# Kernel tuning notes

Hardware: AMD Instinct MI355X
Metric: run time of the kernel (lower is better)

## Reference

```python
import jax, jax.numpy as jnp
import numpy as np


def setup_inputs() -> dict:
    key = jax.random.key(0)
    k1, k2 = jax.random.split(key)
    N, D, C = 65536, 512, 64
    embeddings = jax.random.normal(k1, (N, D), dtype=jnp.float32)
    labels = jax.random.randint(k2, (N,), 0, C, dtype=jnp.int64)
    return {"embeddings": embeddings, "labels": labels, "num_classes": C}


def reference(embeddings, labels, num_classes):
    # Per-class mean (prototypes) via segment reductions. Labels are assumed
    # to be 0..C-1 with all classes present, so unique(labels) == arange(C)
    # and local_labels == labels (faithful to the torch loop in that regime).
    ones = jnp.ones(labels.shape, dtype=embeddings.dtype)
    counts = jax.ops.segment_sum(ones, labels, num_segments=num_classes)  # [C]
    sums = jax.ops.segment_sum(embeddings, labels, num_segments=num_classes)  # [C, D]
    prototypes = sums / counts[:, None]

    # Euclidean cdist: ||e||^2 + ||p||^2 - 2 e.p^T, clamped for numerical safety
    e2 = jnp.sum(embeddings * embeddings, axis=1, keepdims=True)  # [N, 1]
    p2 = jnp.sum(prototypes * prototypes, axis=1)  # [C]
    cross = embeddings @ prototypes.T  # [N, C]
    d2 = jnp.maximum(e2 + p2[None, :] - 2.0 * cross, 1e-12)
    logits = -jnp.sqrt(d2)  # [N, C], negative distances

    log_probs = jax.nn.log_softmax(logits, axis=1)
    n = labels.shape[0]
    nll = -log_probs[jnp.arange(n), labels]
    loss = jnp.mean(nll)
    accuracy = jnp.mean((jnp.argmax(logits, axis=1) == labels).astype(jnp.float32))
    return (loss, accuracy)
```

## Files before the change

kernel.cpp:

```cpp
#include <hip/hip_runtime.h>
#include <math.h>

#define NROWS 65536
#define DIM   512
#define NCLS  64
#define CCAP  1280

typedef __attribute__((ext_vector_type(4))) float f32x4;
typedef __attribute__((ext_vector_type(8))) short s16x8;

#define WS_PROTOSUM 0
#define WS_CURSORS  32768
#define WS_LOSS     32832
#define WS_ACC      32833
#define WS_DONE     32834
#define WS_P2       32836
#define WS_PERM     32912
#define WS_PBF      114944
#define WS_E2P      131328
#define WS_EBF      393472
#define WS_EXT_BYTES 68682752ULL
#define MEMSET_WORDS 32835

static __device__ __forceinline__ unsigned short f2bf(float f) {
    unsigned int u = __float_as_uint(f);
    u += 0x7FFF + ((u >> 16) & 1);
    return (unsigned short)(u >> 16);
}
static __device__ __forceinline__ float bf2f(unsigned short h) {
    return __uint_as_float(((unsigned int)h) << 16);
}

__global__ __launch_bounds__(256) void k_scatter(const int* __restrict__ labels,
                                                 int* __restrict__ cursors,
                                                 int* __restrict__ perm) {
    __shared__ int lh[NCLS], lb[NCLS];
    int t = threadIdx.x;
    if (t < NCLS) lh[t] = 0;
    __syncthreads();
    int i = blockIdx.x * 256 + t;
    int lab = labels[i];
    int rank = atomicAdd(&lh[lab], 1);
    __syncthreads();
    if (t < NCLS) lb[t] = atomicAdd(&cursors[t], lh[t]);
    __syncthreads();
    int pos = lb[lab] + rank;
    if (pos < CCAP) perm[lab * CCAP + pos] = i;
}

__global__ __launch_bounds__(256) void k_psumprep(const float* __restrict__ emb,
                                                  const int* __restrict__ cursors,
                                                  const int* __restrict__ perm,
                                                  float* __restrict__ protoSum,
                                                  unsigned short* __restrict__ ebf,
                                                  float* __restrict__ e2p) {
    __shared__ int permS[CCAP];
    __shared__ float4 red[256];
    int t   = threadIdx.x;
    int c   = blockIdx.x >> 5;
    int sub = blockIdx.x & 31;
    int dc  = sub & 3;
    int rs  = sub >> 2;
    int tl  = t & 31;
    int g   = t >> 5;

    int cnt = cursors[c];
    int n = (cnt < CCAP) ? cnt : CCAP;
    for (int i = t; i < n; i += 256) permS[i] = perm[c * CCAP + i];
    __syncthreads();

    const float4* eb = (const float4*)emb + dc * 32 + tl;
    float* e2o = e2p + (size_t)dc * NROWS;
    float4 acc = make_float4(0.f, 0.f, 0.f, 0.f);
#pragma unroll 2
    for (int i = rs * 8 + g; i < n; i += 64) {
        int r = permS[i];
        float4 v = eb[(size_t)r * 128];
        acc.x += v.x; acc.y += v.y; acc.z += v.z; acc.w += v.w;
        ushort4 h;
        h.x = f2bf(v.x); h.y = f2bf(v.y); h.z = f2bf(v.z); h.w = f2bf(v.w);
        *(ushort4*)(ebf + (size_t)r * DIM + dc * 128 + tl * 4) = h;
        float sq = v.x * v.x + v.y * v.y + v.z * v.z + v.w * v.w;
#pragma unroll
        for (int o = 1; o < 32; o <<= 1) sq += __shfl_xor(sq, o, 64);
        if (tl == 0) e2o[r] = sq;
    }
    red[t] = acc;
    __syncthreads();
    if (t < 32) {
        float4 s = red[t];
#pragma unroll
        for (int gg = 1; gg < 8; ++gg) {
            float4 v = red[gg * 32 + t];
            s.x += v.x; s.y += v.y; s.z += v.z; s.w += v.w;
        }
        float* dst = &protoSum[(size_t)c * DIM + dc * 128 + t * 4];
        atomicAdd(dst + 0, s.x);
        atomicAdd(dst + 1, s.y);
        atomicAdd(dst + 2, s.z);
        atomicAdd(dst + 3, s.w);
    }
}

__global__ __launch_bounds__(256) void k_psum(const float* __restrict__ emb,
                                              const int* __restrict__ cursors,
                                              const int* __restrict__ perm,
                                              float* __restrict__ protoSum) {
    __shared__ int permS[CCAP];
    __shared__ float4 red[256];
    int t   = threadIdx.x;
    int c   = blockIdx.x >> 5;
    int sub = blockIdx.x & 31;
    int dc  = sub & 3;
    int rs  = sub >> 2;
    int tl  = t & 31;
    int g   = t >> 5;

    int cnt = cursors[c];
    int n = (cnt < CCAP) ? cnt : CCAP;
    for (int i = t; i < n; i += 256) permS[i] = perm[c * CCAP + i];
    __syncthreads();

    const float4* eb = (const float4*)emb + dc * 32 + tl;
    float4 acc = make_float4(0.f, 0.f, 0.f, 0.f);
#pragma unroll 4
    for (int i = rs * 8 + g; i < n; i += 64) {
        int r = permS[i];
        float4 v = eb[(size_t)r * 128];
        acc.x += v.x; acc.y += v.y; acc.z += v.z; acc.w += v.w;
    }
    red[t] = acc;
    __syncthreads();
    if (t < 32) {
        float4 s = red[t];
#pragma unroll
        for (int gg = 1; gg < 8; ++gg) {
            float4 v = red[gg * 32 + t];
            s.x += v.x; s.y += v.y; s.z += v.z; s.w += v.w;
        }
        float* dst = &protoSum[(size_t)c * DIM + dc * 128 + t * 4];
        atomicAdd(dst + 0, s.x);
        atomicAdd(dst + 1, s.y);
        atomicAdd(dst + 2, s.z);
        atomicAdd(dst + 3, s.w);
    }
}

__global__ __launch_bounds__(512) void k_protofin(const float* __restrict__ protoSum,
                                                  const int* __restrict__ cursors,
                                                  unsigned short* __restrict__ pBf,
                                                  float* __restrict__ p2) {
    int c = blockIdx.x, d = threadIdx.x;
    float mean = protoSum[(size_t)c * DIM + d] / (float)cursors[c];
    unsigned short mb = f2bf(mean);
    int kc = d >> 5, quad = (d >> 3) & 3, j = d & 7;
    int nt = c >> 4, l15 = c & 15;
    pBf[(size_t)(((kc * 4 + quad) * 4 + nt) * 16 + l15) * 8 + j] = mb;
    float mf = bf2f(mb);
    float sq = mf * mf;
#pragma unroll
    for (int o = 32; o > 0; o >>= 1) sq += __shfl_down(sq, o, 64);
    __shared__ float red[8];
    if ((d & 63) == 0) red[d >> 6] = sq;
    __syncthreads();
    if (d == 0) {
        float ss = 0.f;
#pragma unroll
        for (int w = 0; w < 8; ++w) ss += red[w];
        p2[c] = ss;
    }
}

#define LROWS 64
#define LGRID (NROWS / LROWS)

__global__ __launch_bounds__(256, 4) void k_logits2(const unsigned short* __restrict__ ebf,
                                                 const float* __restrict__ e2p,
                                                 const int* __restrict__ labels,
                                                 const unsigned short* __restrict__ pBf,
                                                 const float* __restrict__ p2,
                                                 float* __restrict__ lossAcc,
                                                 float* __restrict__ accAcc,
                                                 unsigned int* __restrict__ doneCnt,
                                                 float* __restrict__ out) {
    __shared__ float rb[8];
    int t    = threadIdx.x;
    int lane = t & 63;
    int wv   = t >> 6;
    int quad = lane >> 4;
    int l15  = lane & 15;
    int rbase = blockIdx.x * LROWS;
    int row   = wv * 16 + l15;

    f32x4 acc[4];
#pragma unroll
    for (int nt = 0; nt < 4; ++nt) acc[nt] = (f32x4){0.f, 0.f, 0.f, 0.f};

    const s16x8* ap = (const s16x8*)(ebf + (size_t)(rbase + row) * DIM) + quad;
    const s16x8* bp = (const s16x8*)pBf + quad * 64 + l15;

#pragma unroll 4
    for (int kc = 0; kc < 16; ++kc) {
        s16x8 a = ap[kc * 4];
#pragma unroll
        for (int nt = 0; nt < 4; ++nt) {
            s16x8 b = bp[(size_t)kc * 256 + nt * 16];
            acc[nt] = __builtin_amdgcn_mfma_f32_16x16x32_bf16(a, b, acc[nt], 0, 0, 0);
        }
    }

    float nlls = 0.f, corr = 0.f;
#pragma unroll
    for (int reg = 0; reg < 4; ++reg) {
        int rloc = wv * 16 + quad * 4 + reg;
        int grow = rbase + rloc;
        float e2v = e2p[grow] + e2p[NROWS + grow]
                  + e2p[2 * NROWS + grow] + e2p[3 * NROWS + grow];
        float lg[4];
#pragma unroll
        for (int nt = 0; nt < 4; ++nt) {
            float d2 = e2v + p2[nt * 16 + l15] - 2.f * acc[nt][reg];
            d2 = fmaxf(d2, 1e-12f);
            lg[nt] = -sqrtf(d2);
        }
        float mv = lg[0]; int mc = l15;
#pragma unroll
        for (int nt = 1; nt < 4; ++nt) {
            int cix = nt * 16 + l15;
            if (lg[nt] > mv) { mv = lg[nt]; mc = cix; }
        }
#pragma unroll
        for (int o = 1; o < 16; o <<= 1) {
            float mo = __shfl_xor(mv, o, 64);
            int   co = __shfl_xor(mc, o, 64);
            if (mo > mv || (mo == mv && co < mc)) { mv = mo; mc = co; }
        }
        int lab = labels[grow];
        float se = 0.f, ll = 0.f;
#pragma unroll
        for (int nt = 0; nt < 4; ++nt) se += __expf(lg[nt] - mv);
        if ((lab & 15) == l15) ll = lg[lab >> 4];
#pragma unroll
        for (int o = 1; o < 16; o <<= 1) {
            se += __shfl_xor(se, o, 64);
            ll += __shfl_xor(ll, o, 64);
        }
        if (l15 == 0) {
            nlls += __logf(se) + mv - ll;
            corr += (mc == lab) ? 1.f : 0.f;
        }
    }
#pragma unroll
    for (int o = 1; o < 64; o <<= 1) {
        nlls += __shfl_xor(nlls, o, 64);
        corr += __shfl_xor(corr, o, 64);
    }
    if (lane == 0) { rb[wv] = nlls; rb[4 + wv] = corr; }
    __syncthreads();
    if (t == 0) {
        atomicAdd(lossAcc, rb[0] + rb[1] + rb[2] + rb[3]);
        atomicAdd(accAcc, rb[4] + rb[5] + rb[6] + rb[7]);
        __threadfence();
        unsigned int tk = atomicAdd(doneCnt, 1u);
        if (tk == LGRID - 1) {
            float ls  = atomicAdd(lossAcc, 0.f);
            float as_ = atomicAdd(accAcc, 0.f);
            out[0] = ls * (1.f / NROWS);
            out[1] = as_ * (1.f / NROWS);
        }
    }
}

__global__ __launch_bounds__(256) void k_logits(const float* __restrict__ emb,
                                                const int* __restrict__ labels,
                                                const unsigned short* __restrict__ pBf,
                                                const float* __restrict__ p2,
                                                float* __restrict__ lossAcc,
                                                float* __restrict__ accAcc,
                                                unsigned int* __restrict__ doneCnt,
                                                float* __restrict__ out) {
    __shared__ float e2s[LROWS];
    __shared__ float rb[8];

    int t    = threadIdx.x;
    int lane = t & 63;
    int wv   = t >> 6;
    int quad = lane >> 4;
    int l15  = lane & 15;
    int rbase = blockIdx.x * LROWS;
    int row   = wv * 16 + l15;

    f32x4 acc[4];
#pragma unroll
    for (int nt = 0; nt < 4; ++nt) acc[nt] = (f32x4){0.f, 0.f, 0.f, 0.f};
    float e2a = 0.f;

    const float4* rp = (const float4*)(emb + (size_t)(rbase + row) * DIM) + quad * 2;
    const s16x8*  bp = (const s16x8*)pBf + quad * 64 + l15;

#pragma unroll 4
    for (int kc = 0; kc < 16; ++kc) {
        float4 g0 = rp[kc * 8];
        float4 g1 = rp[kc * 8 + 1];
        e2a += g0.x * g0.x + g0.y * g0.y + g0.z * g0.z + g0.w * g0.w
             + g1.x * g1.x + g1.y * g1.y + g1.z * g1.z + g1.w * g1.w;
        s16x8 a;
        a[0] = f2bf(g0.x); a[1] = f2bf(g0.y); a[2] = f2bf(g0.z); a[3] = f2bf(g0.w);
        a[4] = f2bf(g1.x); a[5] = f2bf(g1.y); a[6] = f2bf(g1.z); a[7] = f2bf(g1.w);
#pragma unroll
        for (int nt = 0; nt < 4; ++nt) {
            s16x8 b = bp[(size_t)kc * 256 + nt * 16];
            acc[nt] = __builtin_amdgcn_mfma_f32_16x16x32_bf16(a, b, acc[nt], 0, 0, 0);
        }
    }

    e2a += __shfl_xor(e2a, 16, 64);
    e2a += __shfl_xor(e2a, 32, 64);
    if (quad == 0) e2s[row] = e2a;
    __syncthreads();

    float nlls = 0.f, corr = 0.f;
#pragma unroll
    for (int reg = 0; reg < 4; ++reg) {
        int rloc = wv * 16 + quad * 4 + reg;
        float e2v = e2s[rloc];
        float lg[4];
#pragma unroll
        for (int nt = 0; nt < 4; ++nt) {
            float d2 = e2v + p2[nt * 16 + l15] - 2.f * acc[nt][reg];
            d2 = fmaxf(d2, 1e-12f);
            lg[nt] = -sqrtf(d2);
        }
        float mv = lg[0]; int mc = l15;
#pragma unroll
        for (int nt = 1; nt < 4; ++nt) {
            int cix = nt * 16 + l15;
            if (lg[nt] > mv) { mv = lg[nt]; mc = cix; }
        }
#pragma unroll
        for (int o = 1; o < 16; o <<= 1) {
            float mo = __shfl_xor(mv, o, 64);
            int   co = __shfl_xor(mc, o, 64);
            if (mo > mv || (mo == mv && co < mc)) { mv = mo; mc = co; }
        }
        int lab = labels[rbase + rloc];
        float se = 0.f, ll = 0.f;
#pragma unroll
        for (int nt = 0; nt < 4; ++nt) se += __expf(lg[nt] - mv);
        if ((lab & 15) == l15) ll = lg[lab >> 4];
#pragma unroll
        for (int o = 1; o < 16; o <<= 1) {
            se += __shfl_xor(se, o, 64);
            ll += __shfl_xor(ll, o, 64);
        }
        if (l15 == 0) {
            nlls += __logf(se) + mv - ll;
            corr += (mc == lab) ? 1.f : 0.f;
        }
    }
#pragma unroll
    for (int o = 1; o < 64; o <<= 1) {
        nlls += __shfl_xor(nlls, o, 64);
        corr += __shfl_xor(corr, o, 64);
    }
    if (lane == 0) { rb[wv] = nlls; rb[4 + wv] = corr; }
    __syncthreads();
    if (t == 0) {
        atomicAdd(lossAcc, rb[0] + rb[1] + rb[2] + rb[3]);
        atomicAdd(accAcc, rb[4] + rb[5] + rb[6] + rb[7]);
        __threadfence();
        unsigned int tk = atomicAdd(doneCnt, 1u);
        if (tk == LGRID - 1) {
            float ls  = atomicAdd(lossAcc, 0.f);
            float as_ = atomicAdd(accAcc, 0.f);
            out[0] = ls * (1.f / NROWS);
            out[1] = as_ * (1.f / NROWS);
        }
    }
}

extern "C" void kernel_launch(void* const* d_in, const int* in_sizes, int n_in,
                              void* d_out, int out_size, void* d_ws, size_t ws_size,
                              hipStream_t stream) {
    const float* emb    = (const float*)d_in[0];
    const int*   labels = (const int*)d_in[1];
    float* out = (float*)d_out;

    float* wsf = (float*)d_ws;
    int*   wsi = (int*)d_ws;
    float*          protoSum = wsf + WS_PROTOSUM;
    int*            cursors  = wsi + WS_CURSORS;
    float*          lossAcc  = wsf + WS_LOSS;
    float*          accAcc   = wsf + WS_ACC;
    unsigned int*   doneCnt  = (unsigned int*)(wsi + WS_DONE);
    float*          p2       = wsf + WS_P2;
    int*            perm     = wsi + WS_PERM;
    unsigned short* pBf      = (unsigned short*)(wsf + WS_PBF);
    float*          e2p      = wsf + WS_E2P;
    unsigned short* ebf      = (unsigned short*)(wsf + WS_EBF);

    hipMemsetAsync(d_ws, 0, MEMSET_WORDS * sizeof(int), stream);

    k_scatter<<<NROWS / 256, 256, 0, stream>>>(labels, cursors, perm);
    if (ws_size >= WS_EXT_BYTES) {
        k_psumprep<<<NCLS * 32, 256, 0, stream>>>(emb, cursors, perm, protoSum,
                                                  ebf, e2p);
        k_protofin<<<NCLS, 512, 0, stream>>>(protoSum, cursors, pBf, p2);
        k_logits2<<<LGRID, 256, 0, stream>>>(ebf, e2p, labels, pBf, p2,
                                             lossAcc, accAcc, doneCnt, out);
    } else {
        k_psum<<<NCLS * 32, 256, 0, stream>>>(emb, cursors, perm, protoSum);
        k_protofin<<<NCLS, 512, 0, stream>>>(protoSum, cursors, pBf, p2);
        k_logits<<<LGRID, 256, 0, stream>>>(emb, labels, pBf, p2,
                                            lossAcc, accAcc, doneCnt, out);
    }
}
```

Baseline: 279.5 us.

## Split logits kernel class tiles across waves with shared-memory softmax combine

The bf16 MFMA logits kernel now handles 32 rows per block instead of 64. Each row tile is covered by two waves that each compute half of the 64 classes, so there are twice as many blocks and half the accumulators per wave. Per-row max/argmax, sum-exp and label logits are combined across the two class halves through shared memory with two extra barriers. This raises parallelism and occupancy (launch bounds 8) at the cost of extra synchronisation, shared-memory traffic, doubled atomics, and each A row being loaded by two waves.

Result: slower. 365.9 us (+30.9%).

```diff
diff --git a/kernel.cpp b/kernel.cpp
--- a/kernel.cpp
+++ b/kernel.cpp
@@ -171,10 +171,9 @@
     }
 }
 
-#define LROWS 64
-#define LGRID (NROWS / LROWS)
-
-__global__ __launch_bounds__(256, 4) void k_logits2(const unsigned short* __restrict__ ebf,
+#define LROWS2 32
+#define LGRID2 (NROWS / LROWS2)
+__global__ __launch_bounds__(256, 8) void k_logits2(const unsigned short* __restrict__ ebf,
                                                  const float* __restrict__ e2p,
                                                  const int* __restrict__ labels,
                                                  const unsigned short* __restrict__ pBf,
@@ -184,17 +183,24 @@
                                                  unsigned int* __restrict__ doneCnt,
                                                  float* __restrict__ out) {
     __shared__ float rb[8];
+    __shared__ float mxS[2][LROWS2];
+    __shared__ int   mcS[2][LROWS2];
+    __shared__ float seS[2][LROWS2];
+    __shared__ float llS[2][LROWS2];
+
     int t    = threadIdx.x;
     int lane = t & 63;
     int wv   = t >> 6;
+    int rwv  = wv & 1;
+    int cwv  = wv >> 1;
     int quad = lane >> 4;
     int l15  = lane & 15;
-    int rbase = blockIdx.x * LROWS;
-    int row   = wv * 16 + l15;
-
-    f32x4 acc[4];
-#pragma unroll
-    for (int nt = 0; nt < 4; ++nt) acc[nt] = (f32x4){0.f, 0.f, 0.f, 0.f};
+    int rbase = blockIdx.x * LROWS2;
+    int row   = rwv * 16 + l15;
+
+    f32x4 acc[2];
+#pragma unroll
+    for (int nt = 0; nt < 2; ++nt) acc[nt] = (f32x4){0.f, 0.f, 0.f, 0.f};
 
     const s16x8* ap = (const s16x8*)(ebf + (size_t)(rbase + row) * DIM) + quad;
     const s16x8* bp = (const s16x8*)pBf + quad * 64 + l15;
@@ -203,51 +209,71 @@
     for (int kc = 0; kc < 16; ++kc) {
         s16x8 a = ap[kc * 4];
 #pragma unroll
-        for (int nt = 0; nt < 4; ++nt) {
-            s16x8 b = bp[(size_t)kc * 256 + nt * 16];
+        for (int nt = 0; nt < 2; ++nt) {
+            s16x8 b = bp[(size_t)kc * 256 + (cwv * 2 + nt) * 16];
             acc[nt] = __builtin_amdgcn_mfma_f32_16x16x32_bf16(a, b, acc[nt], 0, 0, 0);
         }
     }
 
-    float nlls = 0.f, corr = 0.f;
+    float lgA[4][2];
 #pragma unroll
     for (int reg = 0; reg < 4; ++reg) {
-        int rloc = wv * 16 + quad * 4 + reg;
+        int rloc = rwv * 16 + quad * 4 + reg;
         int grow = rbase + rloc;
         float e2v = e2p[grow] + e2p[NROWS + grow]
                   + e2p[2 * NROWS + grow] + e2p[3 * NROWS + grow];
-        float lg[4];
-#pragma unroll
-        for (int nt = 0; nt < 4; ++nt) {
-            float d2 = e2v + p2[nt * 16 + l15] - 2.f * acc[nt][reg];
+#pragma unroll
+        for (int nt = 0; nt < 2; ++nt) {
+            float d2 = e2v + p2[cwv * 32 + nt * 16 + l15] - 2.f * acc[nt][reg];
             d2 = fmaxf(d2, 1e-12f);
-            lg[nt] = -sqrtf(d2);
-        }
-        float mv = lg[0]; int mc = l15;
-#pragma unroll
-        for (int nt = 1; nt < 4; ++nt) {
-            int cix = nt * 16 + l15;
-            if (lg[nt] > mv) { mv = lg[nt]; mc = cix; }
-        }
+            lgA[reg][nt] = -sqrtf(d2);
+        }
+        float mv = lgA[reg][0]; int mc = cwv * 32 + l15;
+        if (lgA[reg][1] > mv) { mv = lgA[reg][1]; mc = cwv * 32 + 16 + l15; }
 #pragma unroll
         for (int o = 1; o < 16; o <<= 1) {
             float mo = __shfl_xor(mv, o, 64);
             int   co = __shfl_xor(mc, o, 64);
             if (mo > mv || (mo == mv && co < mc)) { mv = mo; mc = co; }
         }
+        if (l15 == 0) { mxS[cwv][rloc] = mv; mcS[cwv][rloc] = mc; }
+    }
+    __syncthreads();
+
+#pragma unroll
+    for (int reg = 0; reg < 4; ++reg) {
+        int rloc = rwv * 16 + quad * 4 + reg;
+        int grow = rbase + rloc;
+        float m0 = mxS[0][rloc], m1 = mxS[1][rloc];
+        float gm = (m1 > m0) ? m1 : m0;
+        float se = __expf(lgA[reg][0] - gm) + __expf(lgA[reg][1] - gm);
         int lab = labels[grow];
-        float se = 0.f, ll = 0.f;
-#pragma unroll
-        for (int nt = 0; nt < 4; ++nt) se += __expf(lg[nt] - mv);
-        if ((lab & 15) == l15) ll = lg[lab >> 4];
+        float ll = 0.f;
+        if ((lab >> 5) == cwv && (lab & 15) == l15) ll = lgA[reg][(lab >> 4) & 1];
 #pragma unroll
         for (int o = 1; o < 16; o <<= 1) {
             se += __shfl_xor(se, o, 64);
             ll += __shfl_xor(ll, o, 64);
         }
-        if (l15 == 0) {
-            nlls += __logf(se) + mv - ll;
-            corr += (mc == lab) ? 1.f : 0.f;
+        if (l15 == 0) { seS[cwv][rloc] = se; llS[cwv][rloc] = ll; }
+    }
+    __syncthreads();
+
+    float nlls = 0.f, corr = 0.f;
+    if (cwv == 0) {
+#pragma unroll
+        for (int reg = 0; reg < 4; ++reg) {
+            int rloc = rwv * 16 + quad * 4 + reg;
+            if (l15 == 0) {
+                float m0 = mxS[0][rloc], m1 = mxS[1][rloc];
+                float gm = (m1 > m0) ? m1 : m0;
+                int   gc = (m1 > m0) ? mcS[1][rloc] : mcS[0][rloc];
+                float se = seS[0][rloc] + seS[1][rloc];
+                float ll = llS[0][rloc] + llS[1][rloc];
+                int lab = labels[rbase + rloc];
+                nlls += __logf(se) + gm - ll;
+                corr += (gc == lab) ? 1.f : 0.f;
+            }
         }
     }
 #pragma unroll
@@ -262,7 +288,7 @@
         atomicAdd(accAcc, rb[4] + rb[5] + rb[6] + rb[7]);
         __threadfence();
         unsigned int tk = atomicAdd(doneCnt, 1u);
-        if (tk == LGRID - 1) {
+        if (tk == LGRID2 - 1) {
             float ls  = atomicAdd(lossAcc, 0.f);
             float as_ = atomicAdd(accAcc, 0.f);
             out[0] = ls * (1.f / NROWS);
@@ -270,6 +296,9 @@
         }
     }
 }
+
+#define LROWS 64
+#define LGRID (NROWS / LROWS)
 
 __global__ __launch_bounds__(256) void k_logits(const float* __restrict__ emb,
                                                 const int* __restrict__ labels,
@@ -406,8 +435,8 @@
         k_psumprep<<<NCLS * 32, 256, 0, stream>>>(emb, cursors, perm, protoSum,
                                                   ebf, e2p);
         k_protofin<<<NCLS, 512, 0, stream>>>(protoSum, cursors, pBf, p2);
-        k_logits2<<<LGRID, 256, 0, stream>>>(ebf, e2p, labels, pBf, p2,
-                                             lossAcc, accAcc, doneCnt, out);
+        k_logits2<<<LGRID2, 256, 0, stream>>>(ebf, e2p, labels, pBf, p2,
+                                              lossAcc, accAcc, doneCnt, out);
     } else {
         k_psum<<<NCLS * 32, 256, 0, stream>>>(emb, cursors, perm, protoSum);
         k_protofin<<<NCLS, 512, 0, stream>>>(protoSum, cursors, pBf, p2);
```
